# Kernel optimization log

Hardware: AMD Instinct MI355X
Metric: run time of the kernel (lower is better)

The kernel has to match this reference:

```python
import jax, jax.numpy as jnp
import numpy as np

EPS = 1e-8


def setup_inputs() -> dict:
    key = jax.random.key(0)
    k1, k2, k3, k4 = jax.random.split(key, 4)
    N, D, P, H = 8192, 512, 128, 128
    x1 = jax.random.normal(k1, (N, D), dtype=jnp.float32)
    proj_w1 = jax.random.normal(k2, (D, D), dtype=jnp.float32) * (1.0 / np.sqrt(D))
    proj_w2 = jax.random.normal(k3, (D, P), dtype=jnp.float32) * (1.0 / np.sqrt(D))
    gc_w = jax.random.normal(k4, (D, H), dtype=jnp.float32) * (1.0 / np.sqrt(D))
    gc_b = jnp.zeros((H,), dtype=jnp.float32)
    return {"x1": x1, "proj_w1": proj_w1, "proj_w2": proj_w2, "gc_w": gc_w, "gc_b": gc_b}


def _cosine_similarity(x):
    # torch.mm(x, x.T) / clamp(||x|| * ||x||.T, eps)
    w = jnp.sqrt(jnp.sum(x * x, axis=1, keepdims=True))  # [N,1]
    return (x @ x.T) / jnp.maximum(w * w.T, EPS)


def reference(x1, proj_w1, proj_w2, gc_w, gc_b):
    # projector: Linear(512,512,bias=False) -> ReLU -> Linear(512,P,bias=False)
    x_proj = jax.nn.relu(x1 @ proj_w1) @ proj_w2  # [N,P]
    # graph build is under @torch.no_grad(): dense fully-connected weighted graph
    A = jax.lax.stop_gradient(_cosine_similarity(x_proj))  # [N,N]
    N = x1.shape[0]
    # WGraphConv (DGL GraphConv w/ edge weights, norm='both'):
    # fully connected graph incl. self loops -> in_degree = N, norm = N^{-1/2} on both sides
    inv_n = jnp.asarray(1.0 / N, dtype=x1.dtype)
    h = x1 @ gc_w            # project first (D > H, cheaper)  [N,H]
    h = (A @ h) * inv_n      # weighted aggregate, symmetric degree norm
    return h + gc_b          # [N,H]
```

## Files before the change

### kernel.cpp

```cpp
#include <hip/hip_runtime.h>
#include <stdint.h>
#include <stddef.h>

typedef short s16x4 __attribute__((ext_vector_type(4)));
typedef short s16x8 __attribute__((ext_vector_type(8)));
typedef float f32x4 __attribute__((ext_vector_type(4)));

#define NN 8192
#define DD 512
#define PP 128
#define HH 128

__device__ __forceinline__ short f2bf(float f) {
  unsigned u = __builtin_bit_cast(unsigned, f);
  u = (u + 0x7fffu + ((u >> 16) & 1u)) >> 16;
  return (short)u;
}

__device__ __forceinline__ void async16(const void* g, void* l) {
  __builtin_amdgcn_global_load_lds(
      (const __attribute__((address_space(1))) unsigned int*)g,
      (__attribute__((address_space(3))) unsigned int*)l, 16, 0, 0);
}

template <int MF>
__device__ __forceinline__ void gemm_core(
    const short* __restrict__ A, long lda,
    const short* __restrict__ BT, long ldb,
    long rowBase, long colBase, int k0, int k1,
    short* As, short* Bs, f32x4 (*acc)[4]) {
  const int tid  = threadIdx.x;
  const int lane = tid & 63;
  const int wid  = tid >> 6;
  const int wr   = (wid >> 1) * (MF * 16);
  const int wc   = (wid & 1) * 64;
  const int srow = lane >> 3;
  const int skk  = (lane & 7) * 8;

  for (int k = k0; k < k1; k += 64) {
#pragma unroll
    for (int it = 0; it < MF; ++it) {
      int r = wid * (MF * 8) + it * 8;
      async16(A + (rowBase + r + srow) * lda + k + skk, As + r * 64);
    }
#pragma unroll
    for (int it = 0; it < 4; ++it) {
      int r = wid * 32 + it * 8;
      async16(BT + (colBase + r + srow) * ldb + k + skk, Bs + r * 64);
    }
    __syncthreads();
#pragma unroll
    for (int ks = 0; ks < 64; ks += 32) {
      s16x8 af[MF], bfv[4];
#pragma unroll
      for (int i = 0; i < MF; ++i)
        af[i]  = *(const s16x8*)(As + (wr + i * 16 + (lane & 15)) * 64 + ks + (lane >> 4) * 8);
#pragma unroll
      for (int i = 0; i < 4; ++i)
        bfv[i] = *(const s16x8*)(Bs + (wc + i * 16 + (lane & 15)) * 64 + ks + (lane >> 4) * 8);
#pragma unroll
      for (int mi = 0; mi < MF; ++mi)
#pragma unroll
        for (int ni = 0; ni < 4; ++ni)
          acc[mi][ni] = __builtin_amdgcn_mfma_f32_16x16x32_bf16(af[mi], bfv[ni], acc[mi][ni], 0, 0, 0);
    }
    __syncthreads();
  }
}

__global__ __launch_bounds__(256) void k_prep(
    const float* __restrict__ x1, const float* __restrict__ w1,
    const float* __restrict__ w2, const float* __restrict__ gcw,
    short* __restrict__ x1b, short* __restrict__ w1t,
    short* __restrict__ w2t, short* __restrict__ gcwt) {
  long b = blockIdx.x;
  int t = threadIdx.x;
  if (b < 4096) {
    long i = b * 256 + t;
    float4 v = ((const float4*)x1)[i];
    s16x4 o;
    o[0] = f2bf(v.x); o[1] = f2bf(v.y); o[2] = f2bf(v.z); o[3] = f2bf(v.w);
    *(s16x4*)(x1b + i * 4) = o;
  } else if (b < 4096 + 1024) {
    long i = (b - 4096) * 256 + t;
    int n = (int)(i >> 9), k = (int)(i & 511);
    w1t[i] = f2bf(w1[(long)k * DD + n]);
  } else if (b < 4096 + 1024 + 256) {
    long i = (b - 5120) * 256 + t;
    int n = (int)(i >> 9), k = (int)(i & 511);
    w2t[i] = f2bf(w2[(long)k * PP + n]);
  } else {
    long i = (b - 5376) * 256 + t;
    int n = (int)(i >> 9), k = (int)(i & 511);
    gcwt[i] = f2bf(gcw[(long)k * HH + n]);
  }
}

__global__ __launch_bounds__(256) void k_g13(const short* __restrict__ x1b,
                                             const short* __restrict__ w1t,
                                             const short* __restrict__ gcwt,
                                             short* __restrict__ Y,
                                             short* __restrict__ hT) {
  __shared__ __align__(16) short As[64 * 64];
  __shared__ __align__(16) short Bs[128 * 64];
  __shared__ __align__(16) short hs[128][66];
  f32x4 acc[2][4];
  f32x4 z = {0.f, 0.f, 0.f, 0.f};
#pragma unroll
  for (int i = 0; i < 2; ++i)
#pragma unroll
    for (int j = 0; j < 4; ++j) acc[i][j] = z;
  const int bx = blockIdx.x;
  const int lane = threadIdx.x & 63, wid = threadIdx.x >> 6;
  const int wr = (wid >> 1) * 32, wc = (wid & 1) * 64;
  if (bx < 512) {
    long rowBase = (long)(bx >> 2) * 64;
    long colBase = (long)(bx & 3) * 128;
    gemm_core<2>(x1b, DD, w1t, DD, rowBase, colBase, 0, DD, As, Bs, acc);
#pragma unroll
    for (int mi = 0; mi < 2; ++mi)
#pragma unroll
      for (int ni = 0; ni < 4; ++ni)
#pragma unroll
        for (int r = 0; r < 4; ++r) {
          long m = rowBase + wr + mi * 16 + ((lane >> 4) << 2) + r;
          long n = colBase + wc + ni * 16 + (lane & 15);
          float v = acc[mi][ni][r];
          Y[m * DD + n] = f2bf(v > 0.f ? v : 0.f);
        }
  } else {
    long rowBase = (long)(bx - 512) * 64;
    gemm_core<2>(x1b, DD, gcwt, DD, rowBase, 0, 0, DD, As, Bs, acc);
#pragma unroll
    for (int mi = 0; mi < 2; ++mi)
#pragma unroll
      for (int ni = 0; ni < 4; ++ni)
#pragma unroll
        for (int r = 0; r < 4; ++r) {
          int mloc = wr + mi * 16 + ((lane >> 4) << 2) + r;
          int n = wc + ni * 16 + (lane & 15);
          hs[n][mloc] = f2bf(acc[mi][ni][r]);
        }
    __syncthreads();
    int t = threadIdx.x;
    int h = t >> 1, m0 = (t & 1) * 32;
#pragma unroll
    for (int j0 = 0; j0 < 32; j0 += 8) {
      s16x8 o;
#pragma unroll
      for (int u = 0; u < 8; ++u) o[u] = hs[h][m0 + j0 + u];
      *(s16x8*)(hT + (long)h * NN + rowBase + m0 + j0) = o;
    }
  }
}

__global__ __launch_bounds__(256) void k_g2(const short* __restrict__ Y,
                                            const short* __restrict__ w2t,
                                            short* __restrict__ xp,
                                            short* __restrict__ xpT,
                                            float* __restrict__ invnw) {
  __shared__ __align__(16) short As[64 * 64];
  __shared__ __align__(16) short Bs[128 * 64];
  __shared__ float xs[64][129];
  __shared__ float invw_s[64];
  f32x4 acc[2][4];
  f32x4 z = {0.f, 0.f, 0.f, 0.f};
#pragma unroll
  for (int i = 0; i < 2; ++i)
#pragma unroll
    for (int j = 0; j < 4; ++j) acc[i][j] = z;
  long rowBase = (long)blockIdx.x * 64;
  gemm_core<2>(Y, DD, w2t, DD, rowBase, 0, 0, DD, As, Bs, acc);
  const int lane = threadIdx.x & 63, wid = threadIdx.x >> 6;
  const int wr = (wid >> 1) * 32, wc = (wid & 1) * 64;
#pragma unroll
  for (int mi = 0; mi < 2; ++mi)
#pragma unroll
    for (int ni = 0; ni < 4; ++ni)
#pragma unroll
      for (int r = 0; r < 4; ++r)
        xs[wr + mi * 16 + ((lane >> 4) << 2) + r][wc + ni * 16 + (lane & 15)] = acc[mi][ni][r];
  __syncthreads();
  int t = threadIdx.x;
  if (t < 64) {
    float s = 0.f;
#pragma unroll 8
    for (int i = 0; i < 128; ++i) { int c = (t + i) & 127; float v = xs[t][c]; s += v * v; }
    float nr = sqrtf(s);
    invnw[rowBase + t] = 1.f / (8192.f * nr);
    invw_s[t] = 1.f / nr;
  }
  __syncthreads();
#pragma unroll
  for (int i = 0; i < 4; ++i) {
    int seg = i * 256 + t;
    int r = seg >> 4, c0 = (seg & 15) * 8;
    s16x8 o;
#pragma unroll
    for (int u = 0; u < 8; ++u) o[u] = f2bf(xs[r][c0 + u]);
    *(s16x8*)(xp + (long)(rowBase + r) * PP + c0) = o;
  }
  int c = t >> 1, n0 = (t & 1) * 32;
#pragma unroll
  for (int j0 = 0; j0 < 32; j0 += 8) {
    s16x8 o;
#pragma unroll
    for (int u = 0; u < 8; ++u) {
      int n = n0 + j0 + u;
      o[u] = f2bf(xs[n][c] * invw_s[n]);
    }
    *(s16x8*)(xpT + (long)c * NN + rowBase + n0 + j0) = o;
  }
}

__global__ __launch_bounds__(256) void k_ge(const short* __restrict__ xpT,
                                            const short* __restrict__ hT,
                                            float* __restrict__ Gp) {
  __shared__ __align__(16) short As[128 * 64];
  __shared__ __align__(16) short Bs[128 * 64];
  f32x4 acc[4][4];
  f32x4 z = {0.f, 0.f, 0.f, 0.f};
#pragma unroll
  for (int i = 0; i < 4; ++i)
#pragma unroll
    for (int j = 0; j < 4; ++j) acc[i][j] = z;
  int s = blockIdx.x;
  gemm_core<4>(xpT, NN, hT, NN, 0, 0, s * 128, s * 128 + 128, As, Bs, acc);
  const int lane = threadIdx.x & 63, wid = threadIdx.x >> 6;
  const int wr = (wid >> 1) * 64, wc = (wid & 1) * 64;
#pragma unroll
  for (int mi = 0; mi < 4; ++mi)
#pragma unroll
    for (int ni = 0; ni < 4; ++ni)
#pragma unroll
      for (int r = 0; r < 4; ++r) {
        int m = wr + mi * 16 + ((lane >> 4) << 2) + r;
        int n = wc + ni * 16 + (lane & 15);
        Gp[(long)s * (PP * HH) + m * HH + n] = acc[mi][ni][r];
      }
}

__global__ __launch_bounds__(256) void k_red(const float* __restrict__ Gp,
                                             short* __restrict__ GT) {
  int i = blockIdx.x * 256 + threadIdx.x;
  float s = 0.f;
#pragma unroll 8
  for (int j = 0; j < 64; ++j) s += Gp[j * (PP * HH) + i];
  int p = i >> 7, h = i & 127;
  GT[h * PP + p] = f2bf(s);
}

__global__ __launch_bounds__(256) void k_gf(const short* __restrict__ xp,
                                            const short* __restrict__ GT,
                                            const float* __restrict__ invnw,
                                            const float* __restrict__ gcb,
                                            float* __restrict__ out) {
  __shared__ __align__(16) short As[64 * 64];
  __shared__ __align__(16) short Bs[128 * 64];
  f32x4 acc[2][4];
  f32x4 z = {0.f, 0.f, 0.f, 0.f};
#pragma unroll
  for (int i = 0; i < 2; ++i)
#pragma unroll
    for (int j = 0; j < 4; ++j) acc[i][j] = z;
  long rowBase = (long)blockIdx.x * 64;
  gemm_core<2>(xp, PP, GT, PP, rowBase, 0, 0, PP, As, Bs, acc);
  const int lane = threadIdx.x & 63, wid = threadIdx.x >> 6;
  const int wr = (wid >> 1) * 32, wc = (wid & 1) * 64;
#pragma unroll
  for (int mi = 0; mi < 2; ++mi)
#pragma unroll
    for (int ni = 0; ni < 4; ++ni)
#pragma unroll
      for (int r = 0; r < 4; ++r) {
        long m = rowBase + wr + mi * 16 + ((lane >> 4) << 2) + r;
        int n = wc + ni * 16 + (lane & 15);
        out[m * HH + n] = acc[mi][ni][r] * invnw[m] + gcb[n];
      }
}

extern "C" void kernel_launch(void* const* d_in, const int* in_sizes, int n_in,
                              void* d_out, int out_size, void* d_ws, size_t ws_size,
                              hipStream_t stream) {
  const float* x1  = (const float*)d_in[0];
  const float* w1  = (const float*)d_in[1];
  const float* w2  = (const float*)d_in[2];
  const float* gcw = (const float*)d_in[3];
  const float* gcb = (const float*)d_in[4];
  float* out = (float*)d_out;

  char* ws = (char*)d_ws;
  size_t off = 0;
  auto alloc = [&](size_t bytes) -> char* {
    char* p = ws + off;
    off += (bytes + 255) & ~(size_t)255;
    return p;
  };
  short* x1b  = (short*)alloc((size_t)NN * DD * 2);
  short* w1t  = (short*)alloc((size_t)DD * DD * 2);
  short* w2t  = (short*)alloc((size_t)PP * DD * 2);
  short* gcwt = (short*)alloc((size_t)HH * DD * 2);
  short* Y    = (short*)alloc((size_t)NN * DD * 2);
  short* xp   = (short*)alloc((size_t)NN * PP * 2);
  short* xpT  = (short*)alloc((size_t)NN * PP * 2);
  short* hT   = (short*)alloc((size_t)NN * HH * 2);
  float* invnw = (float*)alloc((size_t)NN * 4);
  float* Gp   = (float*)alloc((size_t)64 * PP * HH * 4);
  short* GT   = (short*)alloc((size_t)PP * HH * 2);

  hipLaunchKernelGGL(k_prep, dim3(5632), dim3(256), 0, stream,
                     x1, w1, w2, gcw, x1b, w1t, w2t, gcwt);
  hipLaunchKernelGGL(k_g13, dim3(640), dim3(256), 0, stream, x1b, w1t, gcwt, Y, hT);
  hipLaunchKernelGGL(k_g2, dim3(128), dim3(256), 0, stream, Y, w2t, xp, xpT, invnw);
  hipLaunchKernelGGL(k_ge, dim3(64), dim3(256), 0, stream, xpT, hT, Gp);
  hipLaunchKernelGGL(k_red, dim3(64), dim3(256), 0, stream, Gp, GT);
  hipLaunchKernelGGL(k_gf, dim3(128), dim3(256), 0, stream, xp, GT, invnw, gcb, out);
}
```

Baseline: 53.86 us.

## Fuse x1 bf16 conversion into GEMM, tile weight transposes, use atomic G reduction

x1 is no longer converted to bf16 in a separate pass. k_g13 now reads the fp32 input directly, converts it in registers and writes it into an XOR-swizzled LDS tile, with 128x128 tiles per block. The weight transposes now go through an LDS tile so both reads and writes are coalesced. The split-K G reduction uses 128 blocks with atomicAdd into a zeroed buffer instead of partial buffers plus a separate reduce kernel. k_gf now loads the transposed G straight into LDS. Together these drop a large intermediate write and read and two launches, at the cost of atomic contention, a memset, and lower parallelism in k_g13.

Result: slower. 71.33 us (+32.4%).

```diff
diff --git a/kernel.cpp b/kernel.cpp
--- a/kernel.cpp
+++ b/kernel.cpp
@@ -68,57 +68,104 @@
   }
 }
 
-__global__ __launch_bounds__(256) void k_prep(
-    const float* __restrict__ x1, const float* __restrict__ w1,
-    const float* __restrict__ w2, const float* __restrict__ gcw,
-    short* __restrict__ x1b, short* __restrict__ w1t,
-    short* __restrict__ w2t, short* __restrict__ gcwt) {
-  long b = blockIdx.x;
-  int t = threadIdx.x;
-  if (b < 4096) {
-    long i = b * 256 + t;
-    float4 v = ((const float4*)x1)[i];
+__global__ __launch_bounds__(256) void k_prep_w(
+    const float* __restrict__ w1, const float* __restrict__ w2,
+    const float* __restrict__ gcw,
+    short* __restrict__ w1t, short* __restrict__ w2t, short* __restrict__ gcwt) {
+  __shared__ float tile[64][65];
+  int b = blockIdx.x, t = threadIdx.x;
+  const float* src; short* dst; int K0, N0, ldn;
+  if (b < 64)      { src = w1;  dst = w1t;  ldn = 512; K0 = (b >> 3) * 64;        N0 = (b & 7) * 64; }
+  else if (b < 80) { int bb = b - 64; src = w2;  dst = w2t;  ldn = 128; K0 = (bb >> 1) * 64; N0 = (bb & 1) * 64; }
+  else             { int bb = b - 80; src = gcw; dst = gcwt; ldn = 128; K0 = (bb >> 1) * 64; N0 = (bb & 1) * 64; }
+#pragma unroll
+  for (int i = 0; i < 4; ++i) {
+    int idx = i * 1024 + t * 4;
+    int row = idx >> 6, col = idx & 63;
+    float4 v = *(const float4*)(src + (long)(K0 + row) * ldn + N0 + col);
+    tile[row][col] = v.x; tile[row][col + 1] = v.y;
+    tile[row][col + 2] = v.z; tile[row][col + 3] = v.w;
+  }
+  __syncthreads();
+#pragma unroll
+  for (int i = 0; i < 4; ++i) {
+    int idx = i * 1024 + t * 4;
+    int n = idx >> 6, k = idx & 63;
     s16x4 o;
-    o[0] = f2bf(v.x); o[1] = f2bf(v.y); o[2] = f2bf(v.z); o[3] = f2bf(v.w);
-    *(s16x4*)(x1b + i * 4) = o;
-  } else if (b < 4096 + 1024) {
-    long i = (b - 4096) * 256 + t;
-    int n = (int)(i >> 9), k = (int)(i & 511);
-    w1t[i] = f2bf(w1[(long)k * DD + n]);
-  } else if (b < 4096 + 1024 + 256) {
-    long i = (b - 5120) * 256 + t;
-    int n = (int)(i >> 9), k = (int)(i & 511);
-    w2t[i] = f2bf(w2[(long)k * PP + n]);
-  } else {
-    long i = (b - 5376) * 256 + t;
-    int n = (int)(i >> 9), k = (int)(i & 511);
-    gcwt[i] = f2bf(gcw[(long)k * HH + n]);
-  }
-}
-
-__global__ __launch_bounds__(256) void k_g13(const short* __restrict__ x1b,
-                                             const short* __restrict__ w1t,
-                                             const short* __restrict__ gcwt,
-                                             short* __restrict__ Y,
-                                             short* __restrict__ hT) {
-  __shared__ __align__(16) short As[64 * 64];
+#pragma unroll
+    for (int u = 0; u < 4; ++u) o[u] = f2bf(tile[k + u][n]);
+    *(s16x4*)(dst + (long)(N0 + n) * DD + K0 + k) = o;
+  }
+}
+
+__global__ __launch_bounds__(256, 2) void k_g13(const float* __restrict__ x1,
+                                                const short* __restrict__ w1t,
+                                                const short* __restrict__ gcwt,
+                                                short* __restrict__ Y,
+                                                short* __restrict__ hT) {
+  __shared__ __align__(16) short As[128 * 64];
   __shared__ __align__(16) short Bs[128 * 64];
-  __shared__ __align__(16) short hs[128][66];
-  f32x4 acc[2][4];
+  __shared__ __align__(16) short hs[128][136];
+  const int tid = threadIdx.x, lane = tid & 63, wid = tid >> 6;
+  const int wr = (wid >> 1) * 64, wc = (wid & 1) * 64;
+  const int srow = lane >> 3, skk = (lane & 7) * 8;
+  const int bx = blockIdx.x;
+  const bool isG1 = bx < 256;
+  const long rowBase = isG1 ? (long)(bx >> 2) * 128 : (long)(bx - 256) * 128;
+  const long colBase = isG1 ? (long)(bx & 3) * 128 : 0;
+  const short* BT = isG1 ? w1t : gcwt;
+
+  f32x4 acc[4][4];
   f32x4 z = {0.f, 0.f, 0.f, 0.f};
 #pragma unroll
-  for (int i = 0; i < 2; ++i)
+  for (int i = 0; i < 4; ++i)
 #pragma unroll
     for (int j = 0; j < 4; ++j) acc[i][j] = z;
-  const int bx = blockIdx.x;
-  const int lane = threadIdx.x & 63, wid = threadIdx.x >> 6;
-  const int wr = (wid >> 1) * 32, wc = (wid & 1) * 64;
-  if (bx < 512) {
-    long rowBase = (long)(bx >> 2) * 64;
-    long colBase = (long)(bx & 3) * 128;
-    gemm_core<2>(x1b, DD, w1t, DD, rowBase, colBase, 0, DD, As, Bs, acc);
-#pragma unroll
-    for (int mi = 0; mi < 2; ++mi)
+
+  for (int k = 0; k < DD; k += 64) {
+#pragma unroll
+    for (int i = 0; i < 4; ++i) {
+      int s = tid + i * 256;
+      int row = s >> 3, c0 = (s & 7) * 8;
+      const float* g = x1 + (rowBase + row) * DD + k + c0;
+      float4 a = *(const float4*)g;
+      float4 b = *(const float4*)(g + 4);
+      s16x8 o;
+      o[0] = f2bf(a.x); o[1] = f2bf(a.y); o[2] = f2bf(a.z); o[3] = f2bf(a.w);
+      o[4] = f2bf(b.x); o[5] = f2bf(b.y); o[6] = f2bf(b.z); o[7] = f2bf(b.w);
+      int byte = ((row * 64 + c0) * 2) ^ ((row & 7) << 4);
+      *(s16x8*)((char*)As + byte) = o;
+    }
+#pragma unroll
+    for (int it = 0; it < 4; ++it) {
+      int r = wid * 32 + it * 8;
+      async16(BT + (colBase + r + srow) * DD + k + skk, Bs + r * 64);
+    }
+    __syncthreads();
+#pragma unroll
+    for (int ks = 0; ks < 64; ks += 32) {
+      s16x8 af[4], bfv[4];
+#pragma unroll
+      for (int i = 0; i < 4; ++i) {
+        int row = wr + i * 16 + (lane & 15);
+        int byte = ((row * 64 + ks + (lane >> 4) * 8) * 2) ^ ((row & 7) << 4);
+        af[i] = *(const s16x8*)((char*)As + byte);
+      }
+#pragma unroll
+      for (int i = 0; i < 4; ++i)
+        bfv[i] = *(const s16x8*)(Bs + (wc + i * 16 + (lane & 15)) * 64 + ks + (lane >> 4) * 8);
+#pragma unroll
+      for (int mi = 0; mi < 4; ++mi)
+#pragma unroll
+        for (int ni = 0; ni < 4; ++ni)
+          acc[mi][ni] = __builtin_amdgcn_mfma_f32_16x16x32_bf16(af[mi], bfv[ni], acc[mi][ni], 0, 0, 0);
+    }
+    __syncthreads();
+  }
+
+  if (isG1) {
+#pragma unroll
+    for (int mi = 0; mi < 4; ++mi)
 #pragma unroll
       for (int ni = 0; ni < 4; ++ni)
 #pragma unroll
@@ -129,23 +176,20 @@
           Y[m * DD + n] = f2bf(v > 0.f ? v : 0.f);
         }
   } else {
-    long rowBase = (long)(bx - 512) * 64;
-    gemm_core<2>(x1b, DD, gcwt, DD, rowBase, 0, 0, DD, As, Bs, acc);
-#pragma unroll
-    for (int mi = 0; mi < 2; ++mi)
+#pragma unroll
+    for (int mi = 0; mi < 4; ++mi)
 #pragma unroll
       for (int ni = 0; ni < 4; ++ni)
 #pragma unroll
         for (int r = 0; r < 4; ++r) {
-          int mloc = wr + mi * 16 + ((lane >> 4) << 2) + r;
+          int m = wr + mi * 16 + ((lane >> 4) << 2) + r;
           int n = wc + ni * 16 + (lane & 15);
-          hs[n][mloc] = f2bf(acc[mi][ni][r]);
+          hs[n][m] = f2bf(acc[mi][ni][r]);
         }
     __syncthreads();
-    int t = threadIdx.x;
-    int h = t >> 1, m0 = (t & 1) * 32;
-#pragma unroll
-    for (int j0 = 0; j0 < 32; j0 += 8) {
+    int h = tid >> 1, m0 = (tid & 1) * 64;
+#pragma unroll
+    for (int j0 = 0; j0 < 64; j0 += 8) {
       s16x8 o;
 #pragma unroll
       for (int u = 0; u < 8; ++u) o[u] = hs[h][m0 + j0 + u];
@@ -215,7 +259,7 @@
 
 __global__ __launch_bounds__(256) void k_ge(const short* __restrict__ xpT,
                                             const short* __restrict__ hT,
-                                            float* __restrict__ Gp) {
+                                            float* __restrict__ G) {
   __shared__ __align__(16) short As[128 * 64];
   __shared__ __align__(16) short Bs[128 * 64];
   f32x4 acc[4][4];
@@ -225,7 +269,7 @@
 #pragma unroll
     for (int j = 0; j < 4; ++j) acc[i][j] = z;
   int s = blockIdx.x;
-  gemm_core<4>(xpT, NN, hT, NN, 0, 0, s * 128, s * 128 + 128, As, Bs, acc);
+  gemm_core<4>(xpT, NN, hT, NN, 0, 0, s * 64, s * 64 + 64, As, Bs, acc);
   const int lane = threadIdx.x & 63, wid = threadIdx.x >> 6;
   const int wr = (wid >> 1) * 64, wc = (wid & 1) * 64;
 #pragma unroll
@@ -236,37 +280,59 @@
       for (int r = 0; r < 4; ++r) {
         int m = wr + mi * 16 + ((lane >> 4) << 2) + r;
         int n = wc + ni * 16 + (lane & 15);
-        Gp[(long)s * (PP * HH) + m * HH + n] = acc[mi][ni][r];
+        atomicAdd(G + m * HH + n, acc[mi][ni][r]);
       }
 }
 
-__global__ __launch_bounds__(256) void k_red(const float* __restrict__ Gp,
-                                             short* __restrict__ GT) {
-  int i = blockIdx.x * 256 + threadIdx.x;
-  float s = 0.f;
-#pragma unroll 8
-  for (int j = 0; j < 64; ++j) s += Gp[j * (PP * HH) + i];
-  int p = i >> 7, h = i & 127;
-  GT[h * PP + p] = f2bf(s);
-}
-
 __global__ __launch_bounds__(256) void k_gf(const short* __restrict__ xp,
-                                            const short* __restrict__ GT,
+                                            const float* __restrict__ G,
                                             const float* __restrict__ invnw,
                                             const float* __restrict__ gcb,
                                             float* __restrict__ out) {
-  __shared__ __align__(16) short As[64 * 64];
-  __shared__ __align__(16) short Bs[128 * 64];
+  __shared__ __align__(16) short As[64][136];
+  __shared__ __align__(16) short GTs[128][136];
+  const int t = threadIdx.x;
+  const long rowBase = (long)blockIdx.x * 64;
+#pragma unroll
+  for (int i = 0; i < 4; ++i) {
+    int s = t + i * 256;
+    int row = s >> 4, c0 = (s & 15) * 8;
+    *(s16x8*)&As[row][c0] = *(const s16x8*)(xp + (rowBase + row) * PP + c0);
+  }
+#pragma unroll
+  for (int i = 0; i < 16; ++i) {
+    int f = t + i * 256;
+    int p = f >> 5, h0 = (f & 31) * 4;
+    float4 g = ((const float4*)G)[f];
+    GTs[h0][p]     = f2bf(g.x);
+    GTs[h0 + 1][p] = f2bf(g.y);
+    GTs[h0 + 2][p] = f2bf(g.z);
+    GTs[h0 + 3][p] = f2bf(g.w);
+  }
+  __syncthreads();
+  const int lane = t & 63, wid = t >> 6;
+  const int wr = (wid >> 1) * 32, wc = (wid & 1) * 64;
   f32x4 acc[2][4];
   f32x4 z = {0.f, 0.f, 0.f, 0.f};
 #pragma unroll
   for (int i = 0; i < 2; ++i)
 #pragma unroll
     for (int j = 0; j < 4; ++j) acc[i][j] = z;
-  long rowBase = (long)blockIdx.x * 64;
-  gemm_core<2>(xp, PP, GT, PP, rowBase, 0, 0, PP, As, Bs, acc);
-  const int lane = threadIdx.x & 63, wid = threadIdx.x >> 6;
-  const int wr = (wid >> 1) * 32, wc = (wid & 1) * 64;
+#pragma unroll
+  for (int ks = 0; ks < 4; ++ks) {
+    s16x8 af[2], bfv[4];
+#pragma unroll
+    for (int i = 0; i < 2; ++i)
+      af[i] = *(const s16x8*)&As[wr + i * 16 + (lane & 15)][ks * 32 + (lane >> 4) * 8];
+#pragma unroll
+    for (int i = 0; i < 4; ++i)
+      bfv[i] = *(const s16x8*)&GTs[wc + i * 16 + (lane & 15)][ks * 32 + (lane >> 4) * 8];
+#pragma unroll
+    for (int mi = 0; mi < 2; ++mi)
+#pragma unroll
+      for (int ni = 0; ni < 4; ++ni)
+        acc[mi][ni] = __builtin_amdgcn_mfma_f32_16x16x32_bf16(af[mi], bfv[ni], acc[mi][ni], 0, 0, 0);
+  }
 #pragma unroll
   for (int mi = 0; mi < 2; ++mi)
 #pragma unroll
@@ -296,7 +362,6 @@
     off += (bytes + 255) & ~(size_t)255;
     return p;
   };
-  short* x1b  = (short*)alloc((size_t)NN * DD * 2);
   short* w1t  = (short*)alloc((size_t)DD * DD * 2);
   short* w2t  = (short*)alloc((size_t)PP * DD * 2);
   short* gcwt = (short*)alloc((size_t)HH * DD * 2);
@@ -305,14 +370,12 @@
   short* xpT  = (short*)alloc((size_t)NN * PP * 2);
   short* hT   = (short*)alloc((size_t)NN * HH * 2);
   float* invnw = (float*)alloc((size_t)NN * 4);
-  float* Gp   = (float*)alloc((size_t)64 * PP * HH * 4);
-  short* GT   = (short*)alloc((size_t)PP * HH * 2);
-
-  hipLaunchKernelGGL(k_prep, dim3(5632), dim3(256), 0, stream,
-                     x1, w1, w2, gcw, x1b, w1t, w2t, gcwt);
-  hipLaunchKernelGGL(k_g13, dim3(640), dim3(256), 0, stream, x1b, w1t, gcwt, Y, hT);
+  float* G    = (float*)alloc((size_t)PP * HH * 4);
+
+  hipMemsetAsync(G, 0, (size_t)PP * HH * 4, stream);
+  hipLaunchKernelGGL(k_prep_w, dim3(96), dim3(256), 0, stream, w1, w2, gcw, w1t, w2t, gcwt);
+  hipLaunchKernelGGL(k_g13, dim3(320), dim3(256), 0, stream, x1, w1t, gcwt, Y, hT);
   hipLaunchKernelGGL(k_g2, dim3(128), dim3(256), 0, stream, Y, w2t, xp, xpT, invnw);
-  hipLaunchKernelGGL(k_ge, dim3(64), dim3(256), 0, stream, xpT, hT, Gp);
-  hipLaunchKernelGGL(k_red, dim3(64), dim3(256), 0, stream, Gp, GT);
-  hipLaunchKernelGGL(k_gf, dim3(128), dim3(256), 0, stream, xp, GT, invnw, gcb, out);
-}
+  hipLaunchKernelGGL(k_ge, dim3(128), dim3(256), 0, stream, xpT, hT, G);
+  hipLaunchKernelGGL(k_gf, dim3(128), dim3(256), 0, stream, xp, G, invnw, gcb, out);
+}
```
